# Optimization experiments

Hardware: AMD Instinct MI355X
Metric: run time of the kernel (lower is better)

## Reference

```python
import jax, jax.numpy as jnp
import numpy as np

N = 8192
IN_F = 256
OUT_F = 128
ALPHA = 0.2  # LeakyReLU negative slope
NEG = -1e12


def setup_inputs() -> dict:
    key = jax.random.key(0)
    k1, k2, k3, k4, k5, k6 = jax.random.split(key, 6)
    inp = jax.random.normal(k1, (N, IN_F), dtype=jnp.float32)
    adj = jax.random.randint(k2, (N, N), 0, 2, dtype=jnp.int32)
    # xavier_uniform with gain=1.414
    def xavier(k, shape, gain=1.414):
        fan_in, fan_out = shape[0], shape[1]
        bound = gain * np.sqrt(6.0 / (fan_in + fan_out))
        return jax.random.uniform(k, shape, jnp.float32, -bound, bound)
    W = xavier(k3, (IN_F, OUT_F))
    a = xavier(k4, (2 * OUT_F, 1))
    W_2 = xavier(k5, (IN_F, OUT_F))
    a_2 = xavier(k6, (2 * OUT_F, 1))
    return {"inp": inp, "adj": adj, "W": W, "a": a, "W_2": W_2, "a_2": a_2}


def _gat_head(h, a_vec, mask):
    # Equivalent to e[i,j] = leakyrelu(a^T [h_i ; h_j]) without N^2*2F concat:
    # split a into source/destination halves.
    a_src = a_vec[:OUT_F, 0]   # [F]
    a_dst = a_vec[OUT_F:, 0]   # [F]
    e = (h @ a_src)[:, None] + (h @ a_dst)[None, :]        # [N, N]
    e = jnp.where(e > 0, e, ALPHA * e)                      # LeakyReLU
    e = jnp.where(mask, e, NEG)
    att = jax.nn.softmax(e, axis=1)                         # [N, N]
    # dropout omitted (eval mode, training=False)
    return att @ h                                          # [N, F]


def reference(inp, adj, W, a, W_2, a_2):
    h = inp @ W      # [N, F]
    h_2 = inp @ W_2  # [N, F]
    mask = adj > 0   # adj is nonneg ints so adj*adj>0 is the same mask
    h_prime = _gat_head(h, a, mask)
    h_prime_2 = _gat_head(h_2, a_2, mask)
    h_total = h_prime + 0.5 * h_prime_2
    return jax.nn.elu(h_total)  # concat=True
```

## Files before the change

### kernel.cpp

```cpp
#include <hip/hip_runtime.h>
#include <hip/hip_fp16.h>

#define NN 8192
#define INF 256
#define OUTF 128
#define LOG2E 1.44269504088896340736f

typedef float f32x4 __attribute__((ext_vector_type(4)));
typedef float f32x16 __attribute__((ext_vector_type(16)));
typedef __fp16 h16x8 __attribute__((ext_vector_type(8)));
typedef __fp16 h16x4 __attribute__((ext_vector_type(4)));
typedef __fp16 h16x2 __attribute__((ext_vector_type(2)));
typedef int i32x4 __attribute__((ext_vector_type(4)));

__device__ __forceinline__ void gload_lds16(const void* g, void* l) {
  __builtin_amdgcn_global_load_lds(
      (const __attribute__((address_space(1))) unsigned int*)g,
      (__attribute__((address_space(3))) unsigned int*)l, 16, 0, 0);
}

__device__ __forceinline__ unsigned encf(float f) {
  int b = __float_as_int(f);
  return b >= 0 ? ((unsigned)b | 0x80000000u) : ~(unsigned)b;
}
__device__ __forceinline__ float decf(unsigned u) {
  int b = (u & 0x80000000u) ? (int)(u & 0x7FFFFFFFu) : ~(int)u;
  return __int_as_float(b);
}

__global__ __launch_bounds__(256) void k0_wt(const float* __restrict__ W1,
                                             const float* __restrict__ W2,
                                             __fp16* __restrict__ WT,
                                             unsigned* __restrict__ GMu) {
  if (blockIdx.x == 0 && threadIdx.x < 2) GMu[threadIdx.x] = 0u;
  int m = blockIdx.x * 256 + threadIdx.x;
  int h = m >> 12;
  int r = m & 4095;
  int c = r >> 5;
  int kb = (r >> 1) & 15;
  int hh = r & 1;
  const float* W = h ? W2 : W1;
  float v[8];
#pragma unroll
  for (int s = 0; s < 8; ++s) {
    int koff = 4 * hh + (s & 3) + 8 * (s >> 2);
    v[s] = W[(kb * 16 + koff) * OUTF + c];
  }
  union { h16x2 h2[4]; i32x4 q; } u;
  u.h2[0] = __builtin_amdgcn_cvt_pkrtz(v[0], v[1]);
  u.h2[1] = __builtin_amdgcn_cvt_pkrtz(v[2], v[3]);
  u.h2[2] = __builtin_amdgcn_cvt_pkrtz(v[4], v[5]);
  u.h2[3] = __builtin_amdgcn_cvt_pkrtz(v[6], v[7]);
  *(i32x4*)(WT + (size_t)h * 32768 + c * 256 + kb * 16 + hh * 8) = u.q;
}

__global__ __launch_bounds__(128) void k1_h(
    const float* __restrict__ inp, const __fp16* __restrict__ WT,
    const float* __restrict__ a1, const float* __restrict__ a2,
    __fp16* __restrict__ hT2, float* __restrict__ S, float* __restrict__ D,
    unsigned* __restrict__ GMu) {
  __shared__ __align__(16) float hl[2][32][136];
  int tid = threadIdx.x;
  int w = tid >> 6;
  int l = tid & 63;
  int lr = l & 31, g = l >> 5;
  int i0 = blockIdx.x * 32;
  const __fp16* WTh = WT + (size_t)w * 32768;
  f32x16 acc[4];
#pragma unroll
  for (int nf = 0; nf < 4; ++nf)
#pragma unroll
    for (int e = 0; e < 16; ++e) acc[nf][e] = 0.0f;
  const float* ip = inp + (size_t)(i0 + lr) * INF;
#pragma unroll
  for (int kb = 0; kb < 16; ++kb) {
    f32x4 q0 = *(const f32x4*)(ip + kb * 16 + 4 * g);
    f32x4 q1 = *(const f32x4*)(ip + kb * 16 + 8 + 4 * g);
    union { h16x2 h2[4]; h16x8 h8; } ua;
    ua.h2[0] = __builtin_amdgcn_cvt_pkrtz(q0[0], q0[1]);
    ua.h2[1] = __builtin_amdgcn_cvt_pkrtz(q0[2], q0[3]);
    ua.h2[2] = __builtin_amdgcn_cvt_pkrtz(q1[0], q1[1]);
    ua.h2[3] = __builtin_amdgcn_cvt_pkrtz(q1[2], q1[3]);
#pragma unroll
    for (int nf = 0; nf < 4; ++nf) {
      h16x8 b = *(const h16x8*)(WTh + (nf * 32 + lr) * 256 + kb * 16 + g * 8);
      acc[nf] = __builtin_amdgcn_mfma_f32_32x32x16_f16(ua.h8, b, acc[nf], 0, 0, 0);
    }
  }
#pragma unroll
  for (int nf = 0; nf < 4; ++nf)
#pragma unroll
    for (int r = 0; r < 16; ++r) {
      int row = (r & 3) + 8 * (r >> 2) + 4 * g;
      hl[w][row][nf * 32 + lr] = acc[nf][r];
    }
  __syncthreads();
  const float* av = w ? a2 : a1;
  float s = 0.f, d = 0.f;
#pragma unroll
  for (int cc = 0; cc < 64; cc += 4) {
    int c = g * 64 + cc;
    f32x4 hv = *(const f32x4*)&hl[w][lr][c];
    f32x4 as = *(const f32x4*)(av + c);
    f32x4 ad = *(const f32x4*)(av + 128 + c);
    s += hv[0] * as[0] + hv[1] * as[1] + hv[2] * as[2] + hv[3] * as[3];
    d += hv[0] * ad[0] + hv[1] * ad[1] + hv[2] * ad[2] + hv[3] * ad[3];
  }
  s += __shfl_xor(s, 32);
  d += __shfl_xor(d, 32);
  float dl = d * LOG2E;
  if (g == 0) {
    S[(size_t)w * NN + i0 + lr] = s * LOG2E;
    D[(size_t)w * NN + i0 + lr] = dl;
  }
  float dmax = dl;
#pragma unroll
  for (int off = 1; off < 32; off <<= 1) dmax = fmaxf(dmax, __shfl_xor(dmax, off));
  if (l == 0) atomicMax(GMu + w, encf(dmax));
  __fp16* hTh = hT2 + (size_t)w * (NN * OUTF);
#pragma unroll
  for (int it = 0; it < 8; ++it) {
    int id = it * 64 + l;
    int jb = id >> 8;
    int sub = id & 255;
    int nf = sub >> 6, lq = sub & 63;
    int lqr = lq & 31, lqg = lq >> 5;
    float v[8];
#pragma unroll
    for (int s2 = 0; s2 < 8; ++s2) {
      int kloc = 4 * lqg + (s2 & 3) + 8 * (s2 >> 2);
      v[s2] = hl[w][jb * 16 + kloc][nf * 32 + lqr];
    }
    union { h16x2 h2[4]; i32x4 q; } u2;
    u2.h2[0] = __builtin_amdgcn_cvt_pkrtz(v[0], v[1]);
    u2.h2[1] = __builtin_amdgcn_cvt_pkrtz(v[2], v[3]);
    u2.h2[2] = __builtin_amdgcn_cvt_pkrtz(v[4], v[5]);
    u2.h2[3] = __builtin_amdgcn_cvt_pkrtz(v[6], v[7]);
    *(i32x4*)(hTh + (size_t)((i0 >> 4) + jb) * 2048 + sub * 8) = u2.q;
  }
}

__global__ __launch_bounds__(256, 2) void k2_attn(
    const int* __restrict__ adj, const __fp16* __restrict__ hT2,
    const float* __restrict__ S, const float* __restrict__ D,
    const unsigned* __restrict__ GMu, __fp16* __restrict__ NUM,
    float* __restrict__ DEN) {
  __shared__ __align__(16) char smem[32768];
  __shared__ __align__(16) char maskL[10240];
  int tid = threadIdx.x;
  int w = tid >> 6;
  int l = tid & 63;
  int lr = l & 31, g2 = l >> 5;
  int h = w >> 1, rq = w & 1;
  int rb = blockIdx.x >> 3, js = blockIdx.x & 7;
  int i0 = rb * 128;
  int jwin = js * 1024;
  int base = i0 + rq * 64;
  int row0 = base + lr, row1 = base + 32 + lr;
  float gm = decf(GMu[h]);
  float sf0 = S[(size_t)h * NN + row0];
  float sf1 = S[(size_t)h * NN + row1];
  float t0 = sf0 + gm, t1 = sf1 + gm;
  float cn0 = -fmaxf(t0, 0.2f * t0) - 1000.0f;
  float cn1 = -fmaxf(t1, 0.2f * t1) - 1000.0f;
  float Ac0 = sf0 + cn0, Bc0 = 0.2f * sf0 + cn0;
  float Ac1 = sf1 + cn1, Bc1 = 0.2f * sf1 + cn1;
  const float* Dh = D + (size_t)h * NN + jwin + 4 * g2;

  f32x16 acc[2][4];
#pragma unroll
  for (int f = 0; f < 2; ++f)
#pragma unroll
    for (int nf = 0; nf < 4; ++nf)
#pragma unroll
      for (int e = 0; e < 16; ++e) acc[f][nf][e] = 0.0f;
  float dsum0 = 0.f, dsum1 = 0.f;

  auto STAGE = [&](int jstep, int b) {
#pragma unroll
    for (int q = 0; q < 4; ++q) {
      int kk_l = q >> 1, hh = q & 1;
      const __fp16* gs = hT2 + (size_t)hh * (NN * OUTF) +
                         (size_t)(js * 64 + jstep * 2 + kk_l) * 2048 + tid * 8;
      gload_lds16(gs, smem + b * 16384 + q * 4096 + tid * 16);
    }
  };

  struct Chunk { i32x4 v0, v1, v2, v3; };
  auto LOADC = [&](int c, Chunk& R) {
    int u = c & 7, gg = c >> 3;
    const int* ab = adj + (size_t)(i0 + w * 32 + u * 4) * NN + jwin + gg * 256 + l * 4;
    R.v0 = *(const i32x4*)(ab);
    R.v1 = *(const i32x4*)(ab + NN);
    R.v2 = *(const i32x4*)(ab + 2 * NN);
    R.v3 = *(const i32x4*)(ab + 3 * NN);
  };
  auto BALLOT = [&](int c, const Chunk& R) {
    int u = c & 7, gg = c >> 3;
    char* mrow = maskL + (gg & 1) * 5120 + (w * 32 + u * 4) * 40 + l * 8;
#pragma unroll
    for (int rr = 0; rr < 4; ++rr) {
      i32x4 vv = rr == 0 ? R.v0 : rr == 1 ? R.v1 : rr == 2 ? R.v2 : R.v3;
      unsigned long long b0 = __ballot(vv[0] != 0);
      unsigned long long b1 = __ballot(vv[1] != 0);
      unsigned long long b2 = __ballot(vv[2] != 0);
      unsigned long long b3 = __ballot(vv[3] != 0);
      unsigned long long bsel = b0;
      bsel = (l == 1) ? b1 : bsel;
      bsel = (l == 2) ? b2 : bsel;
      bsel = (l == 3) ? b3 : bsel;
      if (l < 4) *(unsigned long long*)(mrow + rr * 40) = bsel;
    }
  };

  auto MASK32 = [&](int slot, int r, int u) -> unsigned {
    const unsigned char* mb = (const unsigned char*)(maskL + slot * 5120 + r * 40 + u);
    unsigned m0 = mb[0], m1 = mb[8], m2 = mb[16], m3 = mb[24];
    return m0 | (m1 << 8) | (m2 << 16) | (m3 << 24);
  };

  const h16x2 ones = {(__fp16)1.0f, (__fp16)1.0f};
  h16x8 P[2][2];

  auto SOFTMAX = [&](int jstep, int slot, int u) {
    unsigned bts0 = MASK32(slot, rq * 64 + lr, u) >> g2;
    unsigned bts1 = MASK32(slot, rq * 64 + 32 + lr, u) >> g2;
#pragma unroll
    for (int kk = 0; kk < 2; ++kk) {
      int kkg = jstep * 2 + kk;
      f32x4 d0 = *(const f32x4*)(Dh + kkg * 16);
      f32x4 d1 = *(const f32x4*)(Dh + kkg * 16 + 8);
#pragma unroll
      for (int f = 0; f < 2; ++f) {
        float Af = f ? Ac1 : Ac0, Bf_ = f ? Bc1 : Bc0;
        unsigned bts = f ? bts1 : bts0;
        float pv[8];
#pragma unroll
        for (int s = 0; s < 8; ++s) {
          float dd = (s < 4) ? d0[s] : d1[s - 4];
          const int bitp = 8 * (s & 3) + 4 * kk + 2 * (s >> 2);
          float uu = fmaxf(Af + dd, fmaf(0.2f, dd, Bf_));
          float bfv = (float)((bts >> bitp) & 1u);
          pv[s] = __builtin_amdgcn_exp2f(fmaf(bfv, 1000.0f, uu));
        }
        union { h16x2 h2[4]; h16x8 h8; } uq;
        uq.h2[0] = __builtin_amdgcn_cvt_pkrtz(pv[0], pv[1]);
        uq.h2[1] = __builtin_amdgcn_cvt_pkrtz(pv[2], pv[3]);
        uq.h2[2] = __builtin_amdgcn_cvt_pkrtz(pv[4], pv[5]);
        uq.h2[3] = __builtin_amdgcn_cvt_pkrtz(pv[6], pv[7]);
        float ds = f ? dsum1 : dsum0;
#if __has_builtin(__builtin_amdgcn_fdot2)
        ds = __builtin_amdgcn_fdot2(uq.h2[0], ones, ds, false);
        ds = __builtin_amdgcn_fdot2(uq.h2[1], ones, ds, false);
        ds = __builtin_amdgcn_fdot2(uq.h2[2], ones, ds, false);
        ds = __builtin_amdgcn_fdot2(uq.h2[3], ones, ds, false);
#else
        ds += ((pv[0] + pv[1]) + (pv[2] + pv[3])) + ((pv[4] + pv[5]) + (pv[6] + pv[7]));
#endif
        if (f) dsum1 = ds; else dsum0 = ds;
        P[f][kk] = uq.h8;
      }
    }
  };

  auto MFMA_STEP = [&](int b) {
#pragma unroll
    for (int kk = 0; kk < 2; ++kk) {
      const char* lb = smem + b * 16384 + (kk * 2 + h) * 4096 + l * 16;
#pragma unroll
      for (int nf = 0; nf < 4; ++nf) {
        h16x8 Bf = *(const h16x8*)(lb + nf * 1024);
        acc[0][nf] = __builtin_amdgcn_mfma_f32_32x32x16_f16(P[0][kk], Bf, acc[0][nf], 0, 0, 0);
        acc[1][nf] = __builtin_amdgcn_mfma_f32_32x32x16_f16(P[1][kk], Bf, acc[1][nf], 0, 0, 0);
      }
    }
  };

  Chunk RA, RB;
#pragma unroll
  for (int c = 0; c < 8; ++c) { Chunk T; LOADC(c, T); BALLOT(c, T); }
  LOADC(8, RA);
  LOADC(9, RB);
  STAGE(0, 0);
  __syncthreads();

  for (int g = 0; g < 4; ++g) {
#pragma unroll
    for (int u = 0; u < 8; ++u) {
      const int jstep = g * 8 + u;
      const int b = u & 1;
      if (jstep < 31) STAGE(jstep + 1, b ^ 1);
      if (g < 3) {
        if (u & 1) { BALLOT(jstep + 8, RB); if (jstep + 10 < 32) LOADC(jstep + 10, RB); }
        else       { BALLOT(jstep + 8, RA); if (jstep + 10 < 32) LOADC(jstep + 10, RA); }
      }
      SOFTMAX(jstep, g & 1, u);
      MFMA_STEP(b);
      __syncthreads();
    }
  }

  dsum0 += __shfl_xor(dsum0, 32);
  dsum1 += __shfl_xor(dsum1, 32);
  if (g2 == 0) {
    DEN[(size_t)(js * 2 + h) * NN + row0] = dsum0;
    DEN[(size_t)(js * 2 + h) * NN + row1] = dsum1;
  }
#pragma unroll
  for (int f = 0; f < 2; ++f) {
    __fp16* nb = NUM + ((size_t)(js * 2 + h) * NN + base + f * 32) * 128 + lr;
#pragma unroll
    for (int nf = 0; nf < 4; ++nf)
#pragma unroll
      for (int r = 0; r < 16; ++r) {
        int crow = (r & 3) + 8 * (r >> 2) + 4 * g2;
        nb[(size_t)crow * 128 + nf * 32] = (__fp16)acc[f][nf][r];
      }
  }
}

__global__ __launch_bounds__(256) void k3_out(const __fp16* __restrict__ NUM,
                                              const float* __restrict__ DEN,
                                              float* __restrict__ out) {
  int gid = blockIdx.x * 256 + threadIdx.x;
  int i = gid >> 5;
  int c4 = (gid & 31) * 4;
  f32x4 n1 = {0.f, 0.f, 0.f, 0.f}, n2 = {0.f, 0.f, 0.f, 0.f};
  float d1 = 0.f, d2 = 0.f;
#pragma unroll
  for (int js = 0; js < 8; ++js) {
    h16x4 a1v = *(const h16x4*)(NUM + ((size_t)(js * 2 + 0) * NN + i) * 128 + c4);
    h16x4 a2v = *(const h16x4*)(NUM + ((size_t)(js * 2 + 1) * NN + i) * 128 + c4);
#pragma unroll
    for (int e = 0; e < 4; ++e) { n1[e] += (float)a1v[e]; n2[e] += (float)a2v[e]; }
    d1 += DEN[(size_t)(js * 2 + 0) * NN + i];
    d2 += DEN[(size_t)(js * 2 + 1) * NN + i];
  }
  float r1 = 1.0f / d1, r2 = 0.5f / d2;
  f32x4 o;
#pragma unroll
  for (int e = 0; e < 4; ++e) {
    float x = n1[e] * r1 + n2[e] * r2;
    o[e] = x > 0.f ? x : (exp2f(x * LOG2E) - 1.0f);
  }
  *(f32x4*)(out + (size_t)i * 128 + c4) = o;
}

extern "C" void kernel_launch(void* const* d_in, const int* in_sizes, int n_in,
                              void* d_out, int out_size, void* d_ws, size_t ws_size,
                              hipStream_t stream) {
  const float* inp = (const float*)d_in[0];
  const int* adj = (const int*)d_in[1];
  const float* W1 = (const float*)d_in[2];
  const float* a1 = (const float*)d_in[3];
  const float* W2 = (const float*)d_in[4];
  const float* a2 = (const float*)d_in[5];
  float* out = (float*)d_out;
  char* ws = (char*)d_ws;
  __fp16* WT = (__fp16*)(ws);
  __fp16* hT2 = (__fp16*)(ws + 131072);
  float* S = (float*)(ws + 4325376);
  float* D = (float*)(ws + 4390912);
  unsigned* GMu = (unsigned*)(ws + 4456448);
  __fp16* NUM = (__fp16*)(ws + 12845312);
  float* DEN = (float*)(ws + 46399744);

  k0_wt<<<dim3(32), dim3(256), 0, stream>>>(W1, W2, WT, GMu);
  k1_h<<<dim3(256), dim3(128), 0, stream>>>(inp, WT, a1, a2, hT2, S, D, GMu);
  k2_attn<<<dim3(512), dim3(256), 0, stream>>>(adj, hT2, S, D, GMu, NUM, DEN);
  k3_out<<<dim3(1024), dim3(256), 0, stream>>>(NUM, DEN, out);
}
```

Baseline: 117.5 us.

## Load attention B operand directly to registers instead of LDS staging

Removes the LDS double-buffer staging of the fp16 hT operand and has each wave load its B fragments straight from global memory into registers before the MFMA step. This lets the per-step __syncthreads be dropped, keeping only one barrier per group of 8 steps for the mask buffer. The prologue mask loads are also software-pipelined. In exchange, each B tile is now read from global/L2 by both waves sharing a head instead of once per block, register pressure rises by 8 vector registers of B, and global load latency is exposed with no prefetch distance.

Measured after the change: 199.3 us. 1.7x slower.

```diff
diff --git a/kernel.cpp b/kernel.cpp
--- a/kernel.cpp
+++ b/kernel.cpp
@@ -12,12 +12,6 @@
 typedef __fp16 h16x4 __attribute__((ext_vector_type(4)));
 typedef __fp16 h16x2 __attribute__((ext_vector_type(2)));
 typedef int i32x4 __attribute__((ext_vector_type(4)));
-
-__device__ __forceinline__ void gload_lds16(const void* g, void* l) {
-  __builtin_amdgcn_global_load_lds(
-      (const __attribute__((address_space(1))) unsigned int*)g,
-      (__attribute__((address_space(3))) unsigned int*)l, 16, 0, 0);
-}
 
 __device__ __forceinline__ unsigned encf(float f) {
   int b = __float_as_int(f);
@@ -145,7 +139,6 @@
     const float* __restrict__ S, const float* __restrict__ D,
     const unsigned* __restrict__ GMu, __fp16* __restrict__ NUM,
     float* __restrict__ DEN) {
-  __shared__ __align__(16) char smem[32768];
   __shared__ __align__(16) char maskL[10240];
   int tid = threadIdx.x;
   int w = tid >> 6;
@@ -176,13 +169,13 @@
       for (int e = 0; e < 16; ++e) acc[f][nf][e] = 0.0f;
   float dsum0 = 0.f, dsum1 = 0.f;
 
-  auto STAGE = [&](int jstep, int b) {
-#pragma unroll
-    for (int q = 0; q < 4; ++q) {
-      int kk_l = q >> 1, hh = q & 1;
-      const __fp16* gs = hT2 + (size_t)hh * (NN * OUTF) +
-                         (size_t)(js * 64 + jstep * 2 + kk_l) * 2048 + tid * 8;
-      gload_lds16(gs, smem + b * 16384 + q * 4096 + tid * 16);
+  const __fp16* Bbase = hT2 + (size_t)h * (NN * OUTF) + (size_t)(js * 64) * 2048 + l * 8;
+  h16x8 B[8];
+  auto LOADB = [&](int jstep) {
+#pragma unroll
+    for (int q = 0; q < 8; ++q) {
+      int kk = q >> 2, nf = q & 3;
+      B[q] = *(const h16x8*)(Bbase + (size_t)(jstep * 2 + kk) * 2048 + nf * 512);
     }
   };
 
@@ -263,41 +256,39 @@
     }
   };
 
-  auto MFMA_STEP = [&](int b) {
-#pragma unroll
-    for (int kk = 0; kk < 2; ++kk) {
-      const char* lb = smem + b * 16384 + (kk * 2 + h) * 4096 + l * 16;
+  auto MFMA_STEP = [&]() {
+#pragma unroll
+    for (int kk = 0; kk < 2; ++kk)
 #pragma unroll
       for (int nf = 0; nf < 4; ++nf) {
-        h16x8 Bf = *(const h16x8*)(lb + nf * 1024);
-        acc[0][nf] = __builtin_amdgcn_mfma_f32_32x32x16_f16(P[0][kk], Bf, acc[0][nf], 0, 0, 0);
-        acc[1][nf] = __builtin_amdgcn_mfma_f32_32x32x16_f16(P[1][kk], Bf, acc[1][nf], 0, 0, 0);
+        acc[0][nf] = __builtin_amdgcn_mfma_f32_32x32x16_f16(P[0][kk], B[kk * 4 + nf], acc[0][nf], 0, 0, 0);
+        acc[1][nf] = __builtin_amdgcn_mfma_f32_32x32x16_f16(P[1][kk], B[kk * 4 + nf], acc[1][nf], 0, 0, 0);
       }
-    }
-  };
-
-  Chunk RA, RB;
-#pragma unroll
-  for (int c = 0; c < 8; ++c) { Chunk T; LOADC(c, T); BALLOT(c, T); }
-  LOADC(8, RA);
-  LOADC(9, RB);
-  STAGE(0, 0);
+  };
+
+  Chunk R0, R1;
+  LOADC(0, R0);
+  LOADC(1, R1);
+#pragma unroll
+  for (int c = 0; c < 8; ++c) {
+    if (c & 1) { BALLOT(c, R1); LOADC(c + 2, R1); }
+    else       { BALLOT(c, R0); LOADC(c + 2, R0); }
+  }
   __syncthreads();
 
   for (int g = 0; g < 4; ++g) {
 #pragma unroll
     for (int u = 0; u < 8; ++u) {
       const int jstep = g * 8 + u;
-      const int b = u & 1;
-      if (jstep < 31) STAGE(jstep + 1, b ^ 1);
+      LOADB(jstep);
       if (g < 3) {
-        if (u & 1) { BALLOT(jstep + 8, RB); if (jstep + 10 < 32) LOADC(jstep + 10, RB); }
-        else       { BALLOT(jstep + 8, RA); if (jstep + 10 < 32) LOADC(jstep + 10, RA); }
+        if (u & 1) { BALLOT(jstep + 8, R1); if (g < 2 || u < 6) LOADC(jstep + 10, R1); }
+        else       { BALLOT(jstep + 8, R0); if (g < 2 || u < 6) LOADC(jstep + 10, R0); }
       }
       SOFTMAX(jstep, g & 1, u);
-      MFMA_STEP(b);
-      __syncthreads();
-    }
+      MFMA_STEP();
+    }
+    if (g < 3) __syncthreads();
   }
 
   dsum0 += __shfl_xor(dsum0, 32);
```

## Stage two j-steps per LDS buffer to halve barriers in attention kernel

Applied to the files above, without the earlier changes.

The attention kernel now stages the hT tiles for two consecutive j-steps into each LDS double buffer, which grows shared memory from 32 KB to 64 KB. It then runs two softmax+MFMA steps per __syncthreads, halving the number of barriers. The prologue mask loading is also restructured to pipeline the adjacency chunk loads through two register chunks instead of loading them serially. The larger LDS footprint (about 74 KB per block) may reduce how many blocks fit on each CU, working against the launch_bounds(256,2) target.

Result: slower. 122.5 us (+4.3%).

```diff
diff --git a/kernel.cpp b/kernel.cpp
--- a/kernel.cpp
+++ b/kernel.cpp
@@ -145,7 +145,7 @@
     const float* __restrict__ S, const float* __restrict__ D,
     const unsigned* __restrict__ GMu, __fp16* __restrict__ NUM,
     float* __restrict__ DEN) {
-  __shared__ __align__(16) char smem[32768];
+  __shared__ __align__(16) char smem[65536];
   __shared__ __align__(16) char maskL[10240];
   int tid = threadIdx.x;
   int w = tid >> 6;
@@ -176,13 +176,16 @@
       for (int e = 0; e < 16; ++e) acc[f][nf][e] = 0.0f;
   float dsum0 = 0.f, dsum1 = 0.f;
 
-  auto STAGE = [&](int jstep, int b) {
-#pragma unroll
-    for (int q = 0; q < 4; ++q) {
-      int kk_l = q >> 1, hh = q & 1;
-      const __fp16* gs = hT2 + (size_t)hh * (NN * OUTF) +
-                         (size_t)(js * 64 + jstep * 2 + kk_l) * 2048 + tid * 8;
-      gload_lds16(gs, smem + b * 16384 + q * 4096 + tid * 16);
+  auto STAGE2 = [&](int j0, int b) {
+#pragma unroll
+    for (int jj = 0; jj < 2; ++jj) {
+#pragma unroll
+      for (int q = 0; q < 4; ++q) {
+        int kk_l = q >> 1, hh = q & 1;
+        const __fp16* gs = hT2 + (size_t)hh * (NN * OUTF) +
+                           (size_t)(js * 64 + (j0 + jj) * 2 + kk_l) * 2048 + tid * 8;
+        gload_lds16(gs, smem + b * 32768 + jj * 16384 + q * 4096 + tid * 16);
+      }
     }
   };
 
@@ -263,10 +266,10 @@
     }
   };
 
-  auto MFMA_STEP = [&](int b) {
+  auto MFMA_STEP = [&](int b, int jj) {
 #pragma unroll
     for (int kk = 0; kk < 2; ++kk) {
-      const char* lb = smem + b * 16384 + (kk * 2 + h) * 4096 + l * 16;
+      const char* lb = smem + b * 32768 + jj * 16384 + (kk * 2 + h) * 4096 + l * 16;
 #pragma unroll
       for (int nf = 0; nf < 4; ++nf) {
         h16x8 Bf = *(const h16x8*)(lb + nf * 1024);
@@ -276,28 +279,33 @@
     }
   };
 
-  Chunk RA, RB;
-#pragma unroll
-  for (int c = 0; c < 8; ++c) { Chunk T; LOADC(c, T); BALLOT(c, T); }
-  LOADC(8, RA);
-  LOADC(9, RB);
-  STAGE(0, 0);
+  Chunk R0, R1;
+  LOADC(0, R0);
+  LOADC(1, R1);
+#pragma unroll
+  for (int c = 0; c < 8; ++c) {
+    if (c & 1) { BALLOT(c, R1); LOADC(c + 2, R1); }
+    else       { BALLOT(c, R0); LOADC(c + 2, R0); }
+  }
+  STAGE2(0, 0);
   __syncthreads();
 
-  for (int g = 0; g < 4; ++g) {
-#pragma unroll
-    for (int u = 0; u < 8; ++u) {
-      const int jstep = g * 8 + u;
-      const int b = u & 1;
-      if (jstep < 31) STAGE(jstep + 1, b ^ 1);
-      if (g < 3) {
-        if (u & 1) { BALLOT(jstep + 8, RB); if (jstep + 10 < 32) LOADC(jstep + 10, RB); }
-        else       { BALLOT(jstep + 8, RA); if (jstep + 10 < 32) LOADC(jstep + 10, RA); }
-      }
-      SOFTMAX(jstep, g & 1, u);
-      MFMA_STEP(b);
-      __syncthreads();
-    }
+  for (int gp = 0; gp < 16; ++gp) {
+    const int b = gp & 1;
+    const int g = gp >> 2, qq = gp & 3;
+    const int j0 = gp * 2;
+    if (gp < 15) STAGE2(j0 + 2, b ^ 1);
+    if (g < 3) {
+      int c0 = 8 + g * 8 + 2 * qq;
+      BALLOT(c0, R0);
+      BALLOT(c0 + 1, R1);
+      if (c0 + 3 <= 31) { LOADC(c0 + 2, R0); LOADC(c0 + 3, R1); }
+    }
+    SOFTMAX(j0, g & 1, 2 * qq);
+    MFMA_STEP(b, 0);
+    SOFTMAX(j0 + 1, g & 1, 2 * qq + 1);
+    MFMA_STEP(b, 1);
+    __syncthreads();
   }
 
   dsum0 += __shfl_xor(dsum0, 32);
```

## Triple-buffer attention B tiles with explicit vmcnt waits and stage D in LDS

Applied to the files above, without the earlier changes.

The attention kernel moves from double to triple buffering of the fp16 h tiles in LDS, prefetching two steps ahead. The __syncthreads at the end of each step is replaced by a raw s_barrier preceded by partial vmcnt waits, so later global-to-LDS loads can stay in flight. The D window for both heads is staged into LDS once instead of being read from global memory in every softmax step, and the mask chunk preload is software-pipelined. LDS use grows to about 67KB per block, which may limit occupancy against the 2-blocks launch bound, and the hand-tuned vmcnt counts are fragile if the number of outstanding loads changes.

New measurement: 121.9 us. 3.7% more time.

```diff
diff --git a/kernel.cpp b/kernel.cpp
--- a/kernel.cpp
+++ b/kernel.cpp
@@ -145,8 +145,9 @@
     const float* __restrict__ S, const float* __restrict__ D,
     const unsigned* __restrict__ GMu, __fp16* __restrict__ NUM,
     float* __restrict__ DEN) {
-  __shared__ __align__(16) char smem[32768];
+  __shared__ __align__(16) char smem[49152];
   __shared__ __align__(16) char maskL[10240];
+  __shared__ __align__(16) float Dw[2][1024];
   int tid = threadIdx.x;
   int w = tid >> 6;
   int l = tid & 63;
@@ -165,7 +166,6 @@
   float cn1 = -fmaxf(t1, 0.2f * t1) - 1000.0f;
   float Ac0 = sf0 + cn0, Bc0 = 0.2f * sf0 + cn0;
   float Ac1 = sf1 + cn1, Bc1 = 0.2f * sf1 + cn1;
-  const float* Dh = D + (size_t)h * NN + jwin + 4 * g2;
 
   f32x16 acc[2][4];
 #pragma unroll
@@ -221,6 +221,7 @@
 
   const h16x2 ones = {(__fp16)1.0f, (__fp16)1.0f};
   h16x8 P[2][2];
+  const float* DwH = &Dw[0][0] + h * 1024 + 4 * g2;
 
   auto SOFTMAX = [&](int jstep, int slot, int u) {
     unsigned bts0 = MASK32(slot, rq * 64 + lr, u) >> g2;
@@ -228,8 +229,8 @@
 #pragma unroll
     for (int kk = 0; kk < 2; ++kk) {
       int kkg = jstep * 2 + kk;
-      f32x4 d0 = *(const f32x4*)(Dh + kkg * 16);
-      f32x4 d1 = *(const f32x4*)(Dh + kkg * 16 + 8);
+      f32x4 d0 = *(const f32x4*)(DwH + kkg * 16);
+      f32x4 d1 = *(const f32x4*)(DwH + kkg * 16 + 8);
 #pragma unroll
       for (int f = 0; f < 2; ++f) {
         float Af = f ? Ac1 : Ac0, Bf_ = f ? Bc1 : Bc0;
@@ -276,28 +277,45 @@
     }
   };
 
-  Chunk RA, RB;
-#pragma unroll
-  for (int c = 0; c < 8; ++c) { Chunk T; LOADC(c, T); BALLOT(c, T); }
-  LOADC(8, RA);
-  LOADC(9, RB);
+  Chunk R0, R1;
+  LOADC(0, R0);
+  LOADC(1, R1);
+#pragma unroll
+  for (int c = 0; c < 8; ++c) {
+    if (c & 1) { BALLOT(c, R1); LOADC(c + 2, R1); }
+    else       { BALLOT(c, R0); LOADC(c + 2, R0); }
+  }
+#pragma unroll
+  for (int q = 0; q < 2; ++q) {
+    int idx = q * 256 + tid;
+    int hh = idx >> 8, jj = idx & 255;
+    gload_lds16(D + (size_t)hh * NN + jwin + jj * 4, (char*)&Dw[0][0] + idx * 16);
+  }
   STAGE(0, 0);
-  __syncthreads();
-
-  for (int g = 0; g < 4; ++g) {
-#pragma unroll
-    for (int u = 0; u < 8; ++u) {
-      const int jstep = g * 8 + u;
-      const int b = u & 1;
-      if (jstep < 31) STAGE(jstep + 1, b ^ 1);
-      if (g < 3) {
-        if (u & 1) { BALLOT(jstep + 8, RB); if (jstep + 10 < 32) LOADC(jstep + 10, RB); }
-        else       { BALLOT(jstep + 8, RA); if (jstep + 10 < 32) LOADC(jstep + 10, RA); }
-      }
-      SOFTMAX(jstep, g & 1, u);
-      MFMA_STEP(b);
-      __syncthreads();
-    }
+  STAGE(1, 1);
+  asm volatile("s_waitcnt vmcnt(0) lgkmcnt(0)" ::: "memory");
+  __builtin_amdgcn_s_barrier();
+  __builtin_amdgcn_sched_barrier(0);
+
+  int bcur = 0;
+#pragma unroll 2
+  for (int j = 0; j < 32; ++j) {
+    int bst = bcur + 2; if (bst >= 3) bst -= 3;
+    if (j < 30) STAGE(j + 2, bst);
+    __builtin_amdgcn_sched_barrier(0);
+    if (j < 24) {
+      if (j & 1) { BALLOT(j + 8, R1); if (j < 22) LOADC(j + 10, R1); }
+      else       { BALLOT(j + 8, R0); if (j < 22) LOADC(j + 10, R0); }
+    }
+    __builtin_amdgcn_sched_barrier(0);
+    SOFTMAX(j, (j >> 3) & 1, j & 7);
+    MFMA_STEP(bcur);
+    if (j < 23)      asm volatile("s_waitcnt vmcnt(8) lgkmcnt(0)" ::: "memory");
+    else if (j < 30) asm volatile("s_waitcnt vmcnt(4) lgkmcnt(0)" ::: "memory");
+    else             asm volatile("s_waitcnt vmcnt(0) lgkmcnt(0)" ::: "memory");
+    __builtin_amdgcn_s_barrier();
+    __builtin_amdgcn_sched_barrier(0);
+    bcur = bcur + 1; if (bcur >= 3) bcur = 0;
   }
 
   dsum0 += __shfl_xor(dsum0, 32);
```
